# Kernel optimization log

Hardware: AMD Instinct MI355X
Metric: run time of the kernel (lower is better)

The kernel has to match this reference:

```python
import jax, jax.numpy as jnp
import numpy as np

B, T, C, H = 2, 2048, 1024, 16
Dh = C // H  # 64


def setup_inputs() -> dict:
    key = jax.random.key(0)
    k1, k2, k3 = jax.random.split(key, 3)
    x = jax.random.normal(k1, (B, T, C), dtype=jnp.float32)
    w_attn = jax.random.normal(k2, (C, 3 * C), dtype=jnp.float32) * 0.02
    w_proj = jax.random.normal(k3, (C, C), dtype=jnp.float32) * 0.02
    # precompute_freqs_cis: theta = 10000
    inv_freq = 1.0 / (10000.0 ** (jnp.arange(0, Dh, 2, dtype=jnp.float32) / Dh))  # [Dh/2]
    ang = jnp.arange(T, dtype=jnp.float32)[:, None] * inv_freq[None, :]           # [T, Dh/2]
    return {
        "x": x,
        "w_attn": w_attn,
        "w_proj": w_proj,
        "freqs_cos": jnp.cos(ang),
        "freqs_sin": jnp.sin(ang),
    }


def _apply_rope(t, cos, sin):
    # t: [B, T, H, Dh]; cos/sin: [T, Dh/2] broadcast as [1, T, 1, Dh/2]
    tr = t.reshape(B, T, H, Dh // 2, 2)
    a, b = tr[..., 0], tr[..., 1]  # real, imag parts of complex pairs
    c = cos[None, :, None, :]
    s = sin[None, :, None, :]
    out = jnp.stack([a * c - b * s, a * s + b * c], axis=-1)  # complex multiply
    return out.reshape(B, T, H, Dh)


def reference(x, w_attn, w_proj, freqs_cos, freqs_sin):
    qkv = x @ w_attn                              # [B, T, 3C]
    q, k, v = jnp.split(qkv, 3, axis=-1)
    q = _apply_rope(q.reshape(B, T, H, Dh), freqs_cos, freqs_sin)
    k = _apply_rope(k.reshape(B, T, H, Dh), freqs_cos, freqs_sin)
    v = v.reshape(B, T, H, Dh)
    scale = 1.0 / jnp.sqrt(jnp.float32(Dh))
    scores = jnp.einsum("bqhd,bkhd->bhqk", q, k) * scale  # [B, H, T, T]
    causal = jnp.tril(jnp.ones((T, T), dtype=bool))
    scores = jnp.where(causal[None, None], scores, jnp.float32(-1e30))
    attn = jax.nn.softmax(scores, axis=-1)
    y = jnp.einsum("bhqk,bkhd->bqhd", attn, v).reshape(B, T, C)
    return y @ w_proj
```

## Files before the change

kernel.cpp:

```cpp
#include <hip/hip_runtime.h>

#define TB  2
#define TT  2048
#define TC  1024
#define TH  16
#define TDH 64
#define TN3 3072
#define TM  4096

typedef float f32x4  __attribute__((ext_vector_type(4)));
typedef float f32x16 __attribute__((ext_vector_type(16)));
typedef short bf16x8 __attribute__((ext_vector_type(8)));
typedef short bf16x4 __attribute__((ext_vector_type(4)));
typedef _Float16 f16x8 __attribute__((ext_vector_type(8)));
typedef unsigned short u16x4 __attribute__((ext_vector_type(4)));
typedef unsigned int   u32x4 __attribute__((ext_vector_type(4)));

__device__ __forceinline__ unsigned short f2bf(float x) {
    unsigned u = __builtin_bit_cast(unsigned, x);
    u += 0x7FFF + ((u >> 16) & 1);
    return (unsigned short)(u >> 16);
}
__device__ __forceinline__ unsigned short f2h(float x) {
    return __builtin_bit_cast(unsigned short, (_Float16)x);
}
__device__ __forceinline__ void gload16(const void* g, void* s) {
    __builtin_amdgcn_global_load_lds(
        (const __attribute__((address_space(1))) void*)g,
        (__attribute__((address_space(3))) void*)s, 16, 0, 0);
}

__device__ __forceinline__ void pack8s(const float* p, int hi, unsigned* w) {
    unsigned A, B, C, D;
    asm("v_cvt_pk_bf16_f32 %0, %1, %2" : "=v"(A) : "v"(p[0]), "v"(p[1]));
    asm("v_cvt_pk_bf16_f32 %0, %1, %2" : "=v"(B) : "v"(p[2]), "v"(p[3]));
    asm("v_cvt_pk_bf16_f32 %0, %1, %2" : "=v"(C) : "v"(p[4]), "v"(p[5]));
    asm("v_cvt_pk_bf16_f32 %0, %1, %2" : "=v"(D) : "v"(p[6]), "v"(p[7]));
    const unsigned s0 = hi ? A : C;
    const unsigned s1 = hi ? B : D;
    const unsigned r0 = (unsigned)__shfl_xor((int)s0, 32);
    const unsigned r1 = (unsigned)__shfl_xor((int)s1, 32);
    w[0] = hi ? r0 : A;
    w[1] = hi ? r1 : B;
    w[2] = hi ? C  : r0;
    w[3] = hi ? D  : r1;
}

__global__ __launch_bounds__(256)
void cvt_x(const float* __restrict__ in, unsigned short* __restrict__ of)
{
    const size_t i = ((size_t)blockIdx.x * 256 + threadIdx.x) * 4;
    float4 v = *(const float4*)(in + i);
    ushort4 h;
    h.x = f2h(v.x); h.y = f2h(v.y); h.z = f2h(v.z); h.w = f2h(v.w);
    *(ushort4*)&of[i] = h;
}

__global__ __launch_bounds__(256)
void tcvt(const float* __restrict__ in, unsigned short* __restrict__ of,
          int K, int N)
{
    __shared__ float T[64][65];
    const int k0  = blockIdx.y * 64;
    const int n0t = blockIdx.x * 64;
    const int tid = threadIdx.x;
    const int tr = tid >> 4, tc = tid & 15;
#pragma unroll
    for (int p = 0; p < 4; ++p) {
        const int r = tr + p * 16;
        float4 v = *(const float4*)(in + (size_t)(k0 + r) * N + n0t + tc * 4);
        T[r][tc * 4 + 0] = v.x;
        T[r][tc * 4 + 1] = v.y;
        T[r][tc * 4 + 2] = v.z;
        T[r][tc * 4 + 3] = v.w;
    }
    __syncthreads();
#pragma unroll
    for (int p = 0; p < 4; ++p) {
        const int n = tr + p * 16;
        ushort4 h;
        h.x = f2h(T[tc * 4 + 0][n]);
        h.y = f2h(T[tc * 4 + 1][n]);
        h.z = f2h(T[tc * 4 + 2][n]);
        h.w = f2h(T[tc * 4 + 3][n]);
        *(ushort4*)&of[(size_t)(n0t + n) * K + k0 + tc * 4] = h;
    }
}

template<int EPI>
__global__ __launch_bounds__(256)
void mm_f16(const unsigned short* __restrict__ A, const unsigned short* __restrict__ Bt,
            const float* __restrict__ fcos, const float* __restrict__ fsin,
            unsigned short* __restrict__ qb, unsigned short* __restrict__ kb,
            unsigned short* __restrict__ vb, float* __restrict__ outp)
{
    __shared__ __align__(16) unsigned short LA[4096], LB[4096];

    const int tid = threadIdx.x;
    const int w = tid >> 6, l = tid & 63;
    const int lr = l & 15, lg = l >> 4;
    const int wm = w >> 1, wn = w & 1;
    const int m0 = blockIdx.y * 128, n0 = blockIdx.x * 128;

    const int rA0 = (2 * w) * 16 + (l >> 2);
    const int rA1 = (2 * w + 1) * 16 + (l >> 2);
    const int ksg = ((l & 3) ^ ((l >> 3) & 3)) * 8;

    const unsigned short* pA0 = A + (size_t)(m0 + rA0) * TC + ksg;
    const unsigned short* pA1 = A + (size_t)(m0 + rA1) * TC + ksg;
    const unsigned short* pB0 = Bt + (size_t)(n0 + rA0) * TC + ksg;
    const unsigned short* pB1 = Bt + (size_t)(n0 + rA1) * TC + ksg;

    unsigned short* sA0 = &LA[(2 * w) * 512];
    unsigned short* sA1 = &LA[(2 * w + 1) * 512];
    unsigned short* sB0 = &LB[(2 * w) * 512];
    unsigned short* sB1 = &LB[(2 * w + 1) * 512];

    f32x4 acc[4][4];
#pragma unroll
    for (int i = 0; i < 4; ++i)
#pragma unroll
        for (int j = 0; j < 4; ++j) acc[i][j] = (f32x4){0.f, 0.f, 0.f, 0.f};

    const int kslot = (lg ^ ((lr >> 1) & 3)) * 8;

    for (int kt = 0; kt < TC / 32; ++kt) {
        const int ko = kt * 32;
        gload16(pA0 + ko, sA0);
        gload16(pA1 + ko, sA1);
        gload16(pB0 + ko, sB0);
        gload16(pB1 + ko, sB1);
        __syncthreads();

        f16x8 ah[4], bh[4];
#pragma unroll
        for (int f = 0; f < 4; ++f) {
            const int rowa = wm * 64 + f * 16 + lr;
            const int rowb = wn * 64 + f * 16 + lr;
            ah[f] = *(const f16x8*)&LA[rowa * 32 + kslot];
            bh[f] = *(const f16x8*)&LB[rowb * 32 + kslot];
        }
#pragma unroll
        for (int fm = 0; fm < 4; ++fm)
#pragma unroll
            for (int fn = 0; fn < 4; ++fn)
                acc[fm][fn] = __builtin_amdgcn_mfma_f32_16x16x32_f16(ah[fm], bh[fn], acc[fm][fn], 0, 0, 0);
        __syncthreads();
    }

    if constexpr (EPI == 0) {
#pragma unroll
        for (int fn = 0; fn < 4; ++fn) {
            const int n   = n0 + wn * 64 + fn * 16 + lr;
            const int sec = n >> 10;
            const int hh  = (n & 1023) >> 6;
            const int d   = n & 63;
            unsigned short* dst = (sec == 0) ? qb : ((sec == 1) ? kb : vb);
            const float sc = (sec == 0) ? 0.125f : 1.0f;
            const int dhalf = d >> 1;
#pragma unroll
            for (int fm = 0; fm < 4; ++fm)
#pragma unroll
                for (int r = 0; r < 4; ++r) {
                    const int m  = m0 + wm * 64 + fm * 16 + lg * 4 + r;
                    const int bi = m >> 11;
                    const int t  = m & 2047;
                    const float v = acc[fm][fn][r];
                    const float other = __shfl_xor(v, 1);
                    float outv;
                    if (sec == 2) {
                        outv = v;
                    } else {
                        const float cs = fcos[(size_t)t * (TDH / 2) + dhalf];
                        const float sn = fsin[(size_t)t * (TDH / 2) + dhalf];
                        outv = (lr & 1) ? (other * sn + v * cs) : (v * cs - other * sn);
                    }
                    dst[(((size_t)bi * TH + hh) * TT + t) * TDH + d] = f2bf(outv * sc);
                }
        }
    } else {
#pragma unroll
        for (int fn = 0; fn < 4; ++fn) {
            const int n = n0 + wn * 64 + fn * 16 + lr;
#pragma unroll
            for (int fm = 0; fm < 4; ++fm)
#pragma unroll
                for (int r = 0; r < 4; ++r) {
                    const int m = m0 + wm * 64 + fm * 16 + lg * 4 + r;
                    outp[(size_t)m * TC + n] = acc[fm][fn][r];
                }
        }
    }
}

__global__ __launch_bounds__(64, 2)
void flash_attn(const unsigned short* __restrict__ qb,
                const unsigned short* __restrict__ kb,
                const unsigned short* __restrict__ vb,
                unsigned short* __restrict__ yf)
{
    const int idx = blockIdx.x;
    const int bh  = idx & 31;
    const int qt  = 63 - (idx >> 5);
    const int t0  = qt * 32;
    const int lastkt = qt >> 1;
    const bool qodd = (qt & 1) != 0;
    const int bbT = (bh >> 4) * TT;

    const unsigned short* Qp = qb + (size_t)bh * TT * TDH;
    const unsigned short* Kp = kb + (size_t)bh * TT * TDH;
    const unsigned short* Vp = vb + (size_t)bh * TT * TDH;

    __shared__ __align__(16) unsigned short Vs[2][64 * 64];

    const int l  = threadIdx.x;
    const int lq = l & 31;
    const int hi = l >> 5;

    bf16x8 qf[4];
#pragma unroll
    for (int s = 0; s < 4; ++s)
        qf[s] = *(const bf16x8*)(Qp + (size_t)(t0 + lq) * TDH + s * 16 + hi * 8);

    f32x16 ot[2];
#pragma unroll
    for (int mb = 0; mb < 2; ++mb)
#pragma unroll
        for (int r = 0; r < 16; ++r) ot[mb][r] = 0.f;
    float mrow = -1e30f, lsum = 0.f;

    const unsigned vb0 = (unsigned)(uintptr_t)
        (__attribute__((address_space(3))) unsigned short*)&Vs[0][0];
    const unsigned vlane = vb0 + (unsigned)((hi * 8 + ((l & 15) >> 2)) * 128
                                 + ((l >> 4) & 1) * 32 + (l & 3) * 8);

    const unsigned short* vsrc = Vp + (size_t)(l >> 3) * TDH + (l & 7) * 8;

#define STAGE_V(bufi, ktv)                                                    \
    {                                                                         \
        const unsigned short* s0_ = vsrc + (size_t)(ktv) * 4096;              \
        char* d0_ = (char*)&Vs[bufi][0];                                      \
        _Pragma("unroll")                                                     \
        for (int i_ = 0; i_ < 8; ++i_)                                        \
            gload16(s0_ + i_ * 512, d0_ + i_ * 1024);                         \
    }

    STAGE_V(0, 0);

    bf16x8 kfA[4], kfB[4];
#pragma unroll
    for (int s = 0; s < 4; ++s) {
        kfA[s] = *(const bf16x8*)(Kp + (size_t)lq * TDH + s * 16 + hi * 8);
        kfB[s] = *(const bf16x8*)(Kp + (size_t)(32 + lq) * TDH + s * 16 + hi * 8);
    }

    unsigned pw[4][4];
    bf16x4 trA[2][4], trB[2][4];

    for (int kt = 0; kt < lastkt; ++kt) {
        bf16x8 nA[4], nB[4];
#pragma unroll
        for (int s = 0; s < 4; ++s) {
            nA[s] = *(const bf16x8*)(Kp + (size_t)((kt + 1) * 64 + lq) * TDH + s * 16 + hi * 8);
            nB[s] = *(const bf16x8*)(Kp + (size_t)((kt + 1) * 64 + 32 + lq) * TDH + s * 16 + hi * 8);
        }
        STAGE_V((kt + 1) & 1, kt + 1);

        f32x16 sf0, sf1;
#pragma unroll
        for (int r = 0; r < 16; ++r) { sf0[r] = 0.f; sf1[r] = 0.f; }
#pragma unroll
        for (int s = 0; s < 4; ++s)
            sf0 = __builtin_amdgcn_mfma_f32_32x32x16_bf16(kfA[s], qf[s], sf0, 0, 0, 0);
#pragma unroll
        for (int s = 0; s < 4; ++s)
            sf1 = __builtin_amdgcn_mfma_f32_32x32x16_bf16(kfB[s], qf[s], sf1, 0, 0, 0);

        float tm = -1e30f;
#pragma unroll
        for (int r = 0; r < 16; ++r) tm = fmaxf(tm, fmaxf(sf0[r], sf1[r]));
        tm = fmaxf(tm, __shfl_xor(tm, 32));
        const float mn = fmaxf(mrow, tm);
        const float al = __expf(mrow - mn);
        mrow = mn;
        float rs = 0.f;
#pragma unroll
        for (int r = 0; r < 16; ++r) { sf0[r] = __expf(sf0[r] - mn); rs += sf0[r]; }
#pragma unroll
        for (int r = 0; r < 16; ++r) { sf1[r] = __expf(sf1[r] - mn); rs += sf1[r]; }
        rs += __shfl_xor(rs, 32);
        lsum = lsum * al + rs;
        ot[0] *= al;
        ot[1] *= al;

        {
            float pv[8];
#pragma unroll
            for (int j = 0; j < 8; ++j) pv[j] = sf0[j];
            pack8s(pv, hi, pw[0]);
#pragma unroll
            for (int j = 0; j < 8; ++j) pv[j] = sf0[8 + j];
            pack8s(pv, hi, pw[1]);
#pragma unroll
            for (int j = 0; j < 8; ++j) pv[j] = sf1[j];
            pack8s(pv, hi, pw[2]);
#pragma unroll
            for (int j = 0; j < 8; ++j) pv[j] = sf1[8 + j];
            pack8s(pv, hi, pw[3]);
        }

        asm volatile("s_waitcnt vmcnt(8)" ::: "memory");
        __builtin_amdgcn_sched_barrier(0);
        const unsigned vbb = vlane + (unsigned)((kt & 1) * 8192);
#pragma unroll
        for (int mb = 0; mb < 2; ++mb)
#pragma unroll
            for (int s = 0; s < 4; ++s) {
                const unsigned a0 = vbb + (unsigned)(s * 2048 + mb * 64);
                asm volatile("ds_read_b64_tr_b16 %0, %1" : "=v"(trA[mb][s]) : "v"(a0));
                asm volatile("ds_read_b64_tr_b16 %0, %1" : "=v"(trB[mb][s]) : "v"(a0 + 512));
            }
        asm volatile("s_waitcnt lgkmcnt(0)" ::: "memory");
        __builtin_amdgcn_sched_barrier(0);

#pragma unroll
        for (int mb = 0; mb < 2; ++mb)
#pragma unroll
            for (int s = 0; s < 4; ++s) {
                bf16x8 vf;
#pragma unroll
                for (int j = 0; j < 4; ++j) {
                    vf[j]     = trA[mb][s][j];
                    vf[4 + j] = trB[mb][s][j];
                }
                const bf16x8 pf = __builtin_bit_cast(bf16x8, *(const u32x4*)pw[s]);
                ot[mb] = __builtin_amdgcn_mfma_f32_32x32x16_bf16(vf, pf, ot[mb], 0, 0, 0);
            }

#pragma unroll
        for (int s = 0; s < 4; ++s) { kfA[s] = nA[s]; kfB[s] = nB[s]; }
    }

    {
        const int kt = lastkt;
        f32x16 sf0, sf1;
#pragma unroll
        for (int r = 0; r < 16; ++r) { sf0[r] = 0.f; sf1[r] = 0.f; }
#pragma unroll
        for (int s = 0; s < 4; ++s)
            sf0 = __builtin_amdgcn_mfma_f32_32x32x16_bf16(kfA[s], qf[s], sf0, 0, 0, 0);
        if (qodd) {
#pragma unroll
            for (int s = 0; s < 4; ++s)
                sf1 = __builtin_amdgcn_mfma_f32_32x32x16_bf16(kfB[s], qf[s], sf1, 0, 0, 0);
        }

#pragma unroll
        for (int r = 0; r < 16; ++r) {
            const int crow = (r & 3) + 8 * (r >> 2) + 4 * hi;
            const bool msk = crow > lq;
            if (!qodd) { if (msk) sf0[r] = -1e30f; }
            else       { if (msk) sf1[r] = -1e30f; }
        }

        float tm = -1e30f;
#pragma unroll
        for (int r = 0; r < 16; ++r) tm = fmaxf(tm, sf0[r]);
        if (qodd) {
#pragma unroll
            for (int r = 0; r < 16; ++r) tm = fmaxf(tm, sf1[r]);
        }
        tm = fmaxf(tm, __shfl_xor(tm, 32));
        const float mn = fmaxf(mrow, tm);
        const float al = __expf(mrow - mn);
        mrow = mn;
        float rs = 0.f;
#pragma unroll
        for (int r = 0; r < 16; ++r) { sf0[r] = __expf(sf0[r] - mn); rs += sf0[r]; }
        if (qodd) {
#pragma unroll
            for (int r = 0; r < 16; ++r) { sf1[r] = __expf(sf1[r] - mn); rs += sf1[r]; }
        }
        rs += __shfl_xor(rs, 32);
        lsum = lsum * al + rs;
        ot[0] *= al;
        ot[1] *= al;

        {
            float pv[8];
#pragma unroll
            for (int j = 0; j < 8; ++j) pv[j] = sf0[j];
            pack8s(pv, hi, pw[0]);
#pragma unroll
            for (int j = 0; j < 8; ++j) pv[j] = sf0[8 + j];
            pack8s(pv, hi, pw[1]);
            if (qodd) {
#pragma unroll
                for (int j = 0; j < 8; ++j) pv[j] = sf1[j];
                pack8s(pv, hi, pw[2]);
#pragma unroll
                for (int j = 0; j < 8; ++j) pv[j] = sf1[8 + j];
                pack8s(pv, hi, pw[3]);
            }
        }

        asm volatile("s_waitcnt vmcnt(0)" ::: "memory");
        __builtin_amdgcn_sched_barrier(0);
        const int smax = qodd ? 4 : 2;
        const unsigned vbb = vlane + (unsigned)((kt & 1) * 8192);
#pragma unroll
        for (int mb = 0; mb < 2; ++mb)
#pragma unroll
            for (int s = 0; s < 4; ++s) {
                if (s < smax) {
                    const unsigned a0 = vbb + (unsigned)(s * 2048 + mb * 64);
                    asm volatile("ds_read_b64_tr_b16 %0, %1" : "=v"(trA[mb][s]) : "v"(a0));
                    asm volatile("ds_read_b64_tr_b16 %0, %1" : "=v"(trB[mb][s]) : "v"(a0 + 512));
                }
            }
        asm volatile("s_waitcnt lgkmcnt(0)" ::: "memory");
        __builtin_amdgcn_sched_barrier(0);

#pragma unroll
        for (int mb = 0; mb < 2; ++mb)
#pragma unroll
            for (int s = 0; s < 4; ++s) {
                if (s < smax) {
                    bf16x8 vf;
#pragma unroll
                    for (int j = 0; j < 4; ++j) {
                        vf[j]     = trA[mb][s][j];
                        vf[4 + j] = trB[mb][s][j];
                    }
                    const bf16x8 pf = __builtin_bit_cast(bf16x8, *(const u32x4*)pw[s]);
                    ot[mb] = __builtin_amdgcn_mfma_f32_32x32x16_bf16(vf, pf, ot[mb], 0, 0, 0);
                }
            }
    }

    const float inv = 1.0f / lsum;
    const size_t row = (size_t)(bbT + t0 + lq);
#pragma unroll
    for (int mb = 0; mb < 2; ++mb)
#pragma unroll
        for (int g = 0; g < 4; ++g) {
            u16x4 h4;
#pragma unroll
            for (int j = 0; j < 4; ++j)
                h4[j] = f2h(ot[mb][g * 4 + j] * inv);
            const size_t col = (size_t)((bh & 15) * 64 + mb * 32 + g * 8 + hi * 4);
            *(u16x4*)&yf[row * TC + col] = h4;
        }
#undef STAGE_V
}

extern "C" void kernel_launch(void* const* d_in, const int* in_sizes, int n_in,
                              void* d_out, int out_size, void* d_ws, size_t ws_size,
                              hipStream_t stream)
{
    const float* x      = (const float*)d_in[0];
    const float* w_attn = (const float*)d_in[1];
    const float* w_proj = (const float*)d_in[2];
    const float* fcos   = (const float*)d_in[3];
    const float* fsin   = (const float*)d_in[4];
    float* outp = (float*)d_out;

    const size_t per = (size_t)TB * TH * TT * TDH;
    char* ws = (char*)d_ws;
    unsigned short* qbuf = (unsigned short*)(ws);
    unsigned short* kbuf = qbuf + per;
    unsigned short* vbuf = kbuf + per;
    unsigned short* xf   = vbuf + per;
    unsigned short* waf  = xf + per;
    unsigned short* wpf  = waf + (size_t)TN3 * TC;
    unsigned short* yf   = xf;

    cvt_x<<<dim3(TM * TC / 1024), 256, 0, stream>>>(x, xf);
    tcvt<<<dim3(TN3 / 64, TC / 64), 256, 0, stream>>>(w_attn, waf, TC, TN3);
    tcvt<<<dim3(TC / 64, TC / 64), 256, 0, stream>>>(w_proj, wpf, TC, TC);

    mm_f16<0><<<dim3(TN3 / 128, TM / 128), 256, 0, stream>>>(
        xf, waf, fcos, fsin, qbuf, kbuf, vbuf, nullptr);

    flash_attn<<<dim3(64 * 32), 64, 0, stream>>>(qbuf, kbuf, vbuf, yf);

    mm_f16<1><<<dim3(TC / 128, TM / 128), 256, 0, stream>>>(
        yf, wpf, nullptr, nullptr, nullptr, nullptr, nullptr, outp);
}
```

Before: 239.5 us.

## Double-buffer LDS tiles in f16 GEMM and remap workgroups across XCDs

The GEMM kernel now keeps two LDS stages for A and B tiles. It issues the global-to-LDS loads for the next k-step before computing the current one, so memory latency can overlap with MFMA work and one barrier per iteration goes away. It also remaps the linear workgroup index with a stride-8 permutation, so tiles that share inputs tend to land on the same XCD and improve L2 reuse. The trade-off is doubled LDS use per block, which may reduce occupancy. The remap also assumes the grid size divides by 8.

```diff
diff --git a/kernel.cpp b/kernel.cpp
--- a/kernel.cpp
+++ b/kernel.cpp
@@ -94,13 +94,18 @@
             unsigned short* __restrict__ qb, unsigned short* __restrict__ kb,
             unsigned short* __restrict__ vb, float* __restrict__ outp)
 {
-    __shared__ __align__(16) unsigned short LA[4096], LB[4096];
+    __shared__ __align__(16) unsigned short LA[2][4096], LB[2][4096];
 
     const int tid = threadIdx.x;
     const int w = tid >> 6, l = tid & 63;
     const int lr = l & 15, lg = l >> 4;
     const int wm = w >> 1, wn = w & 1;
-    const int m0 = blockIdx.y * 128, n0 = blockIdx.x * 128;
+
+    const int nwg  = gridDim.x * gridDim.y;
+    const int orig = blockIdx.y * gridDim.x + blockIdx.x;
+    const int wg   = (orig & 7) * (nwg >> 3) + (orig >> 3);
+    const int m0 = (wg / gridDim.x) * 128;
+    const int n0 = (wg % gridDim.x) * 128;
 
     const int rA0 = (2 * w) * 16 + (l >> 2);
     const int rA1 = (2 * w + 1) * 16 + (l >> 2);
@@ -111,10 +116,13 @@
     const unsigned short* pB0 = Bt + (size_t)(n0 + rA0) * TC + ksg;
     const unsigned short* pB1 = Bt + (size_t)(n0 + rA1) * TC + ksg;
 
-    unsigned short* sA0 = &LA[(2 * w) * 512];
-    unsigned short* sA1 = &LA[(2 * w + 1) * 512];
-    unsigned short* sB0 = &LB[(2 * w) * 512];
-    unsigned short* sB1 = &LB[(2 * w + 1) * 512];
+#define MMSTAGE(bufi, ko_)                                          \
+    {                                                               \
+        gload16(pA0 + (ko_), &LA[bufi][(2 * w) * 512]);             \
+        gload16(pA1 + (ko_), &LA[bufi][(2 * w + 1) * 512]);         \
+        gload16(pB0 + (ko_), &LB[bufi][(2 * w) * 512]);             \
+        gload16(pB1 + (ko_), &LB[bufi][(2 * w + 1) * 512]);         \
+    }
 
     f32x4 acc[4][4];
 #pragma unroll
@@ -124,29 +132,30 @@
 
     const int kslot = (lg ^ ((lr >> 1) & 3)) * 8;
 
+    MMSTAGE(0, 0);
+    __syncthreads();
+
     for (int kt = 0; kt < TC / 32; ++kt) {
-        const int ko = kt * 32;
-        gload16(pA0 + ko, sA0);
-        gload16(pA1 + ko, sA1);
-        gload16(pB0 + ko, sB0);
-        gload16(pB1 + ko, sB1);
-        __syncthreads();
+        const int cur = kt & 1;
+        if (kt + 1 < TC / 32) MMSTAGE(cur ^ 1, (kt + 1) * 32);
 
         f16x8 ah[4], bh[4];
 #pragma unroll
         for (int f = 0; f < 4; ++f) {
             const int rowa = wm * 64 + f * 16 + lr;
             const int rowb = wn * 64 + f * 16 + lr;
-            ah[f] = *(const f16x8*)&LA[rowa * 32 + kslot];
-            bh[f] = *(const f16x8*)&LB[rowb * 32 + kslot];
+            ah[f] = *(const f16x8*)&LA[cur][rowa * 32 + kslot];
+            bh[f] = *(const f16x8*)&LB[cur][rowb * 32 + kslot];
         }
 #pragma unroll
         for (int fm = 0; fm < 4; ++fm)
 #pragma unroll
             for (int fn = 0; fn < 4; ++fn)
                 acc[fm][fn] = __builtin_amdgcn_mfma_f32_16x16x32_f16(ah[fm], bh[fn], acc[fm][fn], 0, 0, 0);
+
         __syncthreads();
     }
+#undef MMSTAGE
 
     if constexpr (EPI == 0) {
 #pragma unroll
```

New measurement: 215.7 us. -9.9%, faster.
